# Performance work log

Measured on AMD Instinct MI355X. Metric: run time of the kernel, lower is better.

The kernel has to match this reference:

```python
import jax, jax.numpy as jnp
import numpy as np

B, M, K, D = 16384, 16, 256, 64
T = 1.0


def setup_inputs() -> dict:
    key = jax.random.key(0)
    k1, k2 = jax.random.split(key)
    x = jax.random.normal(k1, (B, M, D), dtype=jnp.float32)
    # nn.init.normal_(self.center, std=0.01)
    center = jax.random.normal(k2, (M, K, D), dtype=jnp.float32) * 0.01
    return {"x": x, "center": center}


def _forward(x, center):
    # x: [B, M, D]; center: [M, K, D]
    x1 = jax.lax.stop_gradient(x)              # x.detach() in the original
    x_sqlen = jnp.sum(x1 * x1, axis=-1)        # [B, M]
    dot = jnp.einsum('mkd,bmd->bmk', center, x1)  # bmm(center, x1) -> [B, M, K]
    c_sqlen = jnp.sum(center * center, axis=-1)   # [M, K]
    dist = c_sqlen[None, :, :] - 2.0 * dot + x_sqlen[:, :, None]  # [B, M, K]
    dist = -jnp.sqrt(dist)
    # softargmax with straight-through estimator
    y_soft = jax.nn.softmax(dist / T, axis=-1)
    label = jnp.argmax(y_soft, axis=-1, keepdims=True)            # [B, M, 1]
    y_hard = jax.nn.one_hot(label[..., 0], K, dtype=dist.dtype)   # [B, M, K]
    assign = y_hard - jax.lax.stop_gradient(y_soft) + y_soft
    # reconstruction: bmm(assign^T(M,B,K), center(M,K,D)) -> [B, M, D]
    recon = jnp.einsum('bmk,mkd->bmd', assign, center)
    return recon, center, label


def reference(x, center):
    return _forward(x, center)
```

## Files before the change

kernel.cpp:

```cpp
#include <hip/hip_runtime.h>
#include <stdint.h>
#include <math.h>

#define B_TOT 16384
#define M_TOT 16
#define K_TOT 256
#define D_TOT 64
#define ROWS_PB 256
#define THREADS 512
#define NCHUNK (B_TOT / ROWS_PB)
#define CAP 2048
#define XERRF 0.0160f
#define SLACK 5.0e-5f

typedef unsigned long long ull;
typedef __attribute__((ext_vector_type(8))) short short8;
typedef __attribute__((ext_vector_type(4))) float f32x4;
typedef __attribute__((ext_vector_type(4))) uint32_t u32x4;

__device__ __forceinline__ uint32_t f32_key(float f) {
  uint32_t u = __float_as_uint(f);
  return (u & 0x80000000u) ? ~u : (u | 0x80000000u);
}
__device__ __forceinline__ ull u64min(ull a, ull b) { return a < b ? a : b; }

__device__ __forceinline__ uint32_t bf16rne(float f) {
  uint32_t u = __float_as_uint(f);
  return (u + 0x7FFFu + ((u >> 16) & 1u)) >> 16;
}
__device__ __forceinline__ uint32_t pack2(float a, float b) {
  return bf16rne(a) | (bf16rne(b) << 16);
}

__device__ __forceinline__ int swz(int row, int c) {
  return row * 128 + ((c * 16) ^ ((row & 7) << 4));
}

__device__ __forceinline__ float xla_hsum16(const float* r) {
#pragma clang fp contract(off)
#pragma clang fp reassociate(off)
  float u[8];
#pragma unroll
  for (int q = 0; q < 8; ++q) u[q] = r[q] + r[q + 8];
  float v[4];
#pragma unroll
  for (int q = 0; q < 4; ++q) v[q] = u[q] + u[q + 4];
  float w0 = v[0] + v[2];
  float w1 = v[1] + v[3];
  return w0 + w1;
}

__device__ __forceinline__ ull exact_key_stream(int k, const float* __restrict__ xrow,
                                                const float* __restrict__ crow,
                                                float csq, float x_sq) {
#pragma clang fp contract(off)
#pragma clang fp reassociate(off)
  const float4* cp = reinterpret_cast<const float4*>(crow);
  const float4* xp = reinterpret_cast<const float4*>(xrow);
  float a[4] = {0.f, 0.f, 0.f, 0.f};
#pragma unroll
  for (int it = 0; it < 4; ++it) {
    float cc[16], xx[16];
#pragma unroll
    for (int q = 0; q < 4; ++q) {
      float4 v = cp[4 * it + q];
      cc[4 * q + 0] = v.x; cc[4 * q + 1] = v.y;
      cc[4 * q + 2] = v.z; cc[4 * q + 3] = v.w;
      float4 w = xp[4 * it + q];
      xx[4 * q + 0] = w.x; xx[4 * q + 1] = w.y;
      xx[4 * q + 2] = w.z; xx[4 * q + 3] = w.w;
    }
#pragma unroll
    for (int L = 0; L < 4; ++L) {
      float m3 = cc[12 + L] * xx[12 + L];
      float s3 = m3 + a[L];
      float m2 = cc[8 + L] * xx[8 + L];
      float s2 = m2 + s3;
      float m1 = cc[4 + L] * xx[4 + L];
      float s1 = m1 + s2;
      float m0 = cc[0 + L] * xx[0 + L];
      a[L] = m0 + s1;
    }
  }
  const float dot = (a[0] + a[1]) + (a[2] + a[3]);
  const float two_dot = 2.0f * dot;
  const float d2 = (csq - two_dot) + x_sq;
  const float s = (float)sqrt((double)d2);
  return (((ull)f32_key(s)) << 32) | (unsigned)k;
}

__global__ __launch_bounds__(THREADS, 4) void mkmeans_fwd(
    const float* __restrict__ x, const float* __restrict__ center,
    float* __restrict__ recon, float* __restrict__ outC, float* __restrict__ outL)
{
#pragma clang fp contract(off)
#pragma clang fp reassociate(off)
  __shared__ __align__(16) char s_xb[ROWS_PB * 128];
  __shared__ __align__(16) char s_cb[K_TOT * 128];
  __shared__ __align__(16) float s_csq[K_TOT];
  __shared__ __align__(16) float s_nch[K_TOT];
  __shared__ float s_xsq[ROWS_PB];
  __shared__ float s_xnorm[ROWS_PB];
  __shared__ float s_cmaxw[4];
  __shared__ ull s_best[ROWS_PB];
  __shared__ uint32_t s_list[CAP];
  __shared__ int s_nc, s_ovf;

  const int t = threadIdx.x;
  const int l = t & 63;
  const int wv = t >> 6;
  const int g = l >> 4;
  const int j = l & 15;
  const int bi = blockIdx.x;
  const int m = bi & (M_TOT - 1);
  const int chunk = bi >> 4;
  const int b0 = chunk * ROWS_PB;

  const float* cmbase = center + (size_t)m * (K_TOT * D_TOT);

  if (t == 0) { s_nc = 0; s_ovf = 0; }

  if (t < ROWS_PB) {
    const float4* xp = reinterpret_cast<const float4*>(
        x + ((size_t)((b0 + t) * M_TOT + m)) * D_TOT);
    float r[16];
#pragma unroll
    for (int mm = 0; mm < 4; ++mm) {
      float q[16];
#pragma unroll
      for (int qq = 0; qq < 4; ++qq) {
        float4 v = xp[4 * mm + qq];
        q[4 * qq + 0] = v.x; q[4 * qq + 1] = v.y;
        q[4 * qq + 2] = v.z; q[4 * qq + 3] = v.w;
      }
#pragma unroll
      for (int jj = 0; jj < 16; ++jj) {
        const float p = q[jj] * q[jj];
        r[jj] = (mm == 0) ? p : (r[jj] + p);
      }
#pragma unroll
      for (int h = 0; h < 2; ++h) {
        u32x4 u = {pack2(q[8 * h + 0], q[8 * h + 1]),
                   pack2(q[8 * h + 2], q[8 * h + 3]),
                   pack2(q[8 * h + 4], q[8 * h + 5]),
                   pack2(q[8 * h + 6], q[8 * h + 7])};
        *reinterpret_cast<u32x4*>(s_xb + swz(t, 2 * mm + h)) = u;
      }
    }
    const float xsq = xla_hsum16(r);
    s_xsq[t] = xsq;
    s_xnorm[t] = sqrtf(xsq) * 1.00001f + 1e-12f;
    s_best[t] = ~0ull;
  } else {
    const int tc = t - ROWS_PB;
    const float4* cp = reinterpret_cast<const float4*>(cmbase + (size_t)tc * D_TOT);
    float4* dst = (chunk == 0)
        ? reinterpret_cast<float4*>(outC + (size_t)m * (K_TOT * D_TOT) + (size_t)tc * D_TOT)
        : nullptr;
    float r[16];
#pragma unroll
    for (int mm = 0; mm < 4; ++mm) {
      float q[16];
#pragma unroll
      for (int qq = 0; qq < 4; ++qq) {
        float4 v = cp[4 * mm + qq];
        if (dst) dst[4 * mm + qq] = v;
        q[4 * qq + 0] = v.x; q[4 * qq + 1] = v.y;
        q[4 * qq + 2] = v.z; q[4 * qq + 3] = v.w;
      }
#pragma unroll
      for (int jj = 0; jj < 16; ++jj) {
        const float p = q[jj] * q[jj];
        r[jj] = (mm == 0) ? p : (r[jj] + p);
      }
#pragma unroll
      for (int h = 0; h < 2; ++h) {
        u32x4 u = {pack2(q[8 * h + 0], q[8 * h + 1]),
                   pack2(q[8 * h + 2], q[8 * h + 3]),
                   pack2(q[8 * h + 4], q[8 * h + 5]),
                   pack2(q[8 * h + 6], q[8 * h + 7])};
        *reinterpret_cast<u32x4*>(s_cb + swz(tc, 2 * mm + h)) = u;
      }
    }
    const float csq = xla_hsum16(r);
    s_csq[tc] = csq;
    s_nch[tc] = -0.5f * csq;
    float cs = sqrtf(csq) * 1.00001f + 1e-12f;
#pragma unroll
    for (int off = 1; off < 64; off <<= 1)
      cs = fmaxf(cs, __shfl_xor(cs, off, 64));
    if (l == 0) s_cmaxw[wv - 4] = cs;
  }
  __syncthreads();

  const int row0 = wv * 32 + j;
  const int row1 = row0 + 16;
  short8 bfr[2][2];
#pragma unroll
  for (int rg = 0; rg < 2; ++rg) {
    const int row = rg ? row1 : row0;
#pragma unroll
    for (int ks = 0; ks < 2; ++ks)
      bfr[rg][ks] = *reinterpret_cast<const short8*>(s_xb + swz(row, ks * 4 + g));
  }
  const float cmax = fmaxf(fmaxf(s_cmaxw[0], s_cmaxw[1]),
                           fmaxf(s_cmaxw[2], s_cmaxw[3]));
  float Wa[2];
  Wa[0] = XERRF * s_xnorm[row0] * cmax + 0.5f * SLACK;
  Wa[1] = XERRF * s_xnorm[row1] * cmax + 0.5f * SLACK;

  float m1[2] = {-3.0e38f, -3.0e38f};
  ull mk[2] = {0ull, 0ull};
#pragma unroll
  for (int T = 0; T < 16; ++T) {
    short8 af0 = *reinterpret_cast<const short8*>(s_cb + swz(T * 16 + j, 0 + g));
    short8 af1 = *reinterpret_cast<const short8*>(s_cb + swz(T * 16 + j, 4 + g));
    const f32x4 nch = *reinterpret_cast<const f32x4*>(&s_nch[T * 16 + g * 4]);
#pragma unroll
    for (int rg = 0; rg < 2; ++rg) {
      f32x4 a = __builtin_amdgcn_mfma_f32_16x16x32_bf16(af0, bfr[rg][0], nch, 0, 0, 0);
      a = __builtin_amdgcn_mfma_f32_16x16x32_bf16(af1, bfr[rg][1], a, 0, 0, 0);
      const float tmax = fmaxf(fmaxf(a[0], a[1]), fmaxf(a[2], a[3]));
      const bool rs = tmax > m1[rg] + Wa[rg];
      const float m1n = fmaxf(m1[rg], tmax);
      const float thr = m1n - Wa[rg];
      uint32_t bits = 0u;
      bits |= (a[0] >= thr) ? 1u : 0u;
      bits |= (a[1] >= thr) ? 2u : 0u;
      bits |= (a[2] >= thr) ? 4u : 0u;
      bits |= (a[3] >= thr) ? 8u : 0u;
      mk[rg] = (rs ? 0ull : mk[rg]) | (((ull)bits) << (4 * T));
      m1[rg] = m1n;
    }
  }

#pragma unroll
  for (int rg = 0; rg < 2; ++rg) {
    float v = m1[rg];
    v = fmaxf(v, __shfl_xor(v, 16, 64));
    v = fmaxf(v, __shfl_xor(v, 32, 64));
    const int row = rg ? row1 : row0;
    if (m1[rg] >= v - Wa[rg]) {
      ull msk = mk[rg];
      while (msk) {
        const int p = __builtin_ctzll(msk);
        msk &= msk - 1;
        const int k = (p >> 2) * 16 + g * 4 + (p & 3);
        const int idx = atomicAdd(&s_nc, 1);
        if (idx < CAP)
          s_list[idx] = ((uint32_t)row << 16) | (uint32_t)k;
        else
          s_ovf = 1;
      }
    }
  }
  __syncthreads();

  if (!s_ovf) {
    const int n = s_nc;
#pragma unroll 1
    for (int i = t; i < n; i += THREADS) {
      const uint32_t e = s_list[i];
      const int row = (int)(e >> 16);
      const int k = (int)(e & 0xffffu);
      const float* xrow = x + ((size_t)((b0 + row) * M_TOT + m)) * D_TOT;
      const float* crow = cmbase + (size_t)k * D_TOT;
      const ull key = exact_key_stream(k, xrow, crow, s_csq[k], s_xsq[row]);
      atomicMin(&s_best[row], key);
    }
  } else if (t < ROWS_PB) {
    const float* xrow = x + ((size_t)((b0 + t) * M_TOT + m)) * D_TOT;
    ull best = ~0ull;
#pragma unroll 1
    for (int k = 0; k < K_TOT; ++k)
      best = u64min(best, exact_key_stream(k, xrow, cmbase + (size_t)k * D_TOT,
                                           s_csq[k], s_xsq[t]));
    s_best[t] = best;
  }
  __syncthreads();

  if (t < ROWS_PB)
    outL[(size_t)(b0 + t) * M_TOT + m] = (float)(uint32_t)(s_best[t] & 0xffffffffull);

  const float4* cm4 = reinterpret_cast<const float4*>(cmbase);
  float4* rec4 = reinterpret_cast<float4*>(recon);
#pragma unroll
  for (int it = 0; it < (ROWS_PB * 16) / THREADS; ++it) {
    const int slot = it * THREADS + t;
    const int row = slot >> 4, ch = slot & 15;
    const int kst = (int)(s_best[row] & 0xffffffffull);
    rec4[((size_t)((b0 + row) * M_TOT + m)) * 16 + ch] = cm4[kst * 16 + ch];
  }
}

extern "C" void kernel_launch(void* const* d_in, const int* in_sizes, int n_in,
                              void* d_out, int out_size, void* d_ws, size_t ws_size,
                              hipStream_t stream) {
  const float* x = (const float*)d_in[0];
  const float* center = (const float*)d_in[1];
  float* recon = (float*)d_out;
  float* outC = recon + (size_t)B_TOT * M_TOT * D_TOT;
  float* outL = outC + (size_t)M_TOT * K_TOT * D_TOT;

  mkmeans_fwd<<<dim3(NCHUNK * M_TOT), dim3(THREADS), 0, stream>>>(x, center, recon, outC, outL);
}
```

Before: 211.2 us.

## Double rows per block, load x fragments from global, filter by per-tile bf16 max

Each block now handles 512 rows instead of 256. The bf16 x staging buffer in shared memory is removed, and each thread loads and packs its MFMA B fragments straight from global memory. The running-max candidate reset is replaced by storing a rounded-up bf16 maximum per 16-key tile, and the candidate list is then filtered per tile against the final row maximum. This is meant to amortize the per-block center staging over more rows and cut LDS traffic. In exchange it uses more registers (occupancy hint drops to 2), reads x from global twice, and may produce more candidates, so CAP is raised.

```diff
diff --git a/kernel.cpp b/kernel.cpp
--- a/kernel.cpp
+++ b/kernel.cpp
@@ -6,10 +6,10 @@
 #define M_TOT 16
 #define K_TOT 256
 #define D_TOT 64
-#define ROWS_PB 256
+#define ROWS_PB 512
 #define THREADS 512
 #define NCHUNK (B_TOT / ROWS_PB)
-#define CAP 2048
+#define CAP 3072
 #define XERRF 0.0160f
 #define SLACK 5.0e-5f
 
@@ -30,6 +30,10 @@
 }
 __device__ __forceinline__ uint32_t pack2(float a, float b) {
   return bf16rne(a) | (bf16rne(b) << 16);
+}
+__device__ __forceinline__ uint32_t bf16up(float f) {
+  uint32_t u = __float_as_uint(f);
+  return (((int)u >= 0) ? (u + 0xFFFFu) : u) >> 16;
 }
 
 __device__ __forceinline__ int swz(int row, int c) {
@@ -89,13 +93,12 @@
   return (((ull)f32_key(s)) << 32) | (unsigned)k;
 }
 
-__global__ __launch_bounds__(THREADS, 4) void mkmeans_fwd(
+__global__ __launch_bounds__(THREADS, 2) void mkmeans_fwd(
     const float* __restrict__ x, const float* __restrict__ center,
     float* __restrict__ recon, float* __restrict__ outC, float* __restrict__ outL)
 {
 #pragma clang fp contract(off)
 #pragma clang fp reassociate(off)
-  __shared__ __align__(16) char s_xb[ROWS_PB * 128];
   __shared__ __align__(16) char s_cb[K_TOT * 128];
   __shared__ __align__(16) float s_csq[K_TOT];
   __shared__ __align__(16) float s_nch[K_TOT];
@@ -119,17 +122,21 @@
   const float* cmbase = center + (size_t)m * (K_TOT * D_TOT);
 
   if (t == 0) { s_nc = 0; s_ovf = 0; }
-
-  if (t < ROWS_PB) {
-    const float4* xp = reinterpret_cast<const float4*>(
-        x + ((size_t)((b0 + t) * M_TOT + m)) * D_TOT);
+  s_best[t] = ~0ull;
+
+  if (t < K_TOT) {
+    const float4* cp = reinterpret_cast<const float4*>(cmbase + (size_t)t * D_TOT);
+    float4* dst = (chunk == 0)
+        ? reinterpret_cast<float4*>(outC + (size_t)m * (K_TOT * D_TOT) + (size_t)t * D_TOT)
+        : nullptr;
     float r[16];
 #pragma unroll
     for (int mm = 0; mm < 4; ++mm) {
       float q[16];
 #pragma unroll
       for (int qq = 0; qq < 4; ++qq) {
-        float4 v = xp[4 * mm + qq];
+        float4 v = cp[4 * mm + qq];
+        if (dst) dst[4 * mm + qq] = v;
         q[4 * qq + 0] = v.x; q[4 * qq + 1] = v.y;
         q[4 * qq + 2] = v.z; q[4 * qq + 3] = v.w;
       }
@@ -144,113 +151,117 @@
                    pack2(q[8 * h + 2], q[8 * h + 3]),
                    pack2(q[8 * h + 4], q[8 * h + 5]),
                    pack2(q[8 * h + 6], q[8 * h + 7])};
-        *reinterpret_cast<u32x4*>(s_xb + swz(t, 2 * mm + h)) = u;
+        *reinterpret_cast<u32x4*>(s_cb + swz(t, 2 * mm + h)) = u;
+      }
+    }
+    const float csq = xla_hsum16(r);
+    s_csq[t] = csq;
+    s_nch[t] = -0.5f * csq;
+    float cs = sqrtf(csq) * 1.00001f + 1e-12f;
+#pragma unroll
+    for (int off = 1; off < 64; off <<= 1)
+      cs = fmaxf(cs, __shfl_xor(cs, off, 64));
+    if (l == 0) s_cmaxw[wv] = cs;
+  }
+
+  {
+    const float4* xp = reinterpret_cast<const float4*>(
+        x + ((size_t)((b0 + t) * M_TOT + m)) * D_TOT);
+    float r[16];
+#pragma unroll
+    for (int mm = 0; mm < 4; ++mm) {
+      float q[16];
+#pragma unroll
+      for (int qq = 0; qq < 4; ++qq) {
+        float4 v = xp[4 * mm + qq];
+        q[4 * qq + 0] = v.x; q[4 * qq + 1] = v.y;
+        q[4 * qq + 2] = v.z; q[4 * qq + 3] = v.w;
+      }
+#pragma unroll
+      for (int jj = 0; jj < 16; ++jj) {
+        const float p = q[jj] * q[jj];
+        r[jj] = (mm == 0) ? p : (r[jj] + p);
       }
     }
     const float xsq = xla_hsum16(r);
     s_xsq[t] = xsq;
     s_xnorm[t] = sqrtf(xsq) * 1.00001f + 1e-12f;
-    s_best[t] = ~0ull;
-  } else {
-    const int tc = t - ROWS_PB;
-    const float4* cp = reinterpret_cast<const float4*>(cmbase + (size_t)tc * D_TOT);
-    float4* dst = (chunk == 0)
-        ? reinterpret_cast<float4*>(outC + (size_t)m * (K_TOT * D_TOT) + (size_t)tc * D_TOT)
-        : nullptr;
-    float r[16];
-#pragma unroll
-    for (int mm = 0; mm < 4; ++mm) {
-      float q[16];
-#pragma unroll
-      for (int qq = 0; qq < 4; ++qq) {
-        float4 v = cp[4 * mm + qq];
-        if (dst) dst[4 * mm + qq] = v;
-        q[4 * qq + 0] = v.x; q[4 * qq + 1] = v.y;
-        q[4 * qq + 2] = v.z; q[4 * qq + 3] = v.w;
-      }
-#pragma unroll
-      for (int jj = 0; jj < 16; ++jj) {
-        const float p = q[jj] * q[jj];
-        r[jj] = (mm == 0) ? p : (r[jj] + p);
-      }
-#pragma unroll
-      for (int h = 0; h < 2; ++h) {
-        u32x4 u = {pack2(q[8 * h + 0], q[8 * h + 1]),
-                   pack2(q[8 * h + 2], q[8 * h + 3]),
-                   pack2(q[8 * h + 4], q[8 * h + 5]),
-                   pack2(q[8 * h + 6], q[8 * h + 7])};
-        *reinterpret_cast<u32x4*>(s_cb + swz(tc, 2 * mm + h)) = u;
-      }
-    }
-    const float csq = xla_hsum16(r);
-    s_csq[tc] = csq;
-    s_nch[tc] = -0.5f * csq;
-    float cs = sqrtf(csq) * 1.00001f + 1e-12f;
-#pragma unroll
-    for (int off = 1; off < 64; off <<= 1)
-      cs = fmaxf(cs, __shfl_xor(cs, off, 64));
-    if (l == 0) s_cmaxw[wv - 4] = cs;
+  }
+
+  short8 bfr[4][2];
+#pragma unroll
+  for (int rg = 0; rg < 4; ++rg) {
+    const int row = wv * 64 + rg * 16 + j;
+    const float4* xr4 = reinterpret_cast<const float4*>(
+        x + ((size_t)((b0 + row) * M_TOT + m)) * D_TOT);
+#pragma unroll
+    for (int ks = 0; ks < 2; ++ks) {
+      const int c = ks * 4 + g;
+      const float4 f0 = xr4[2 * c];
+      const float4 f1 = xr4[2 * c + 1];
+      u32x4 u = {pack2(f0.x, f0.y), pack2(f0.z, f0.w),
+                 pack2(f1.x, f1.y), pack2(f1.z, f1.w)};
+      bfr[rg][ks] = *reinterpret_cast<short8*>(&u);
+    }
   }
   __syncthreads();
 
-  const int row0 = wv * 32 + j;
-  const int row1 = row0 + 16;
-  short8 bfr[2][2];
-#pragma unroll
-  for (int rg = 0; rg < 2; ++rg) {
-    const int row = rg ? row1 : row0;
-#pragma unroll
-    for (int ks = 0; ks < 2; ++ks)
-      bfr[rg][ks] = *reinterpret_cast<const short8*>(s_xb + swz(row, ks * 4 + g));
-  }
   const float cmax = fmaxf(fmaxf(s_cmaxw[0], s_cmaxw[1]),
                            fmaxf(s_cmaxw[2], s_cmaxw[3]));
-  float Wa[2];
-  Wa[0] = XERRF * s_xnorm[row0] * cmax + 0.5f * SLACK;
-  Wa[1] = XERRF * s_xnorm[row1] * cmax + 0.5f * SLACK;
-
-  float m1[2] = {-3.0e38f, -3.0e38f};
-  ull mk[2] = {0ull, 0ull};
+  float Wa[4];
+#pragma unroll
+  for (int rg = 0; rg < 4; ++rg)
+    Wa[rg] = XERRF * s_xnorm[wv * 64 + rg * 16 + j] * cmax + 0.5f * SLACK;
+
+  float m1[4] = {-3.0e38f, -3.0e38f, -3.0e38f, -3.0e38f};
+  ull mk[4] = {0ull, 0ull, 0ull, 0ull};
+  uint32_t tb[4][8];
 #pragma unroll
   for (int T = 0; T < 16; ++T) {
-    short8 af0 = *reinterpret_cast<const short8*>(s_cb + swz(T * 16 + j, 0 + g));
-    short8 af1 = *reinterpret_cast<const short8*>(s_cb + swz(T * 16 + j, 4 + g));
+    const short8 af0 = *reinterpret_cast<const short8*>(s_cb + swz(T * 16 + j, g));
+    const short8 af1 = *reinterpret_cast<const short8*>(s_cb + swz(T * 16 + j, 4 + g));
     const f32x4 nch = *reinterpret_cast<const f32x4*>(&s_nch[T * 16 + g * 4]);
 #pragma unroll
-    for (int rg = 0; rg < 2; ++rg) {
+    for (int rg = 0; rg < 4; ++rg) {
       f32x4 a = __builtin_amdgcn_mfma_f32_16x16x32_bf16(af0, bfr[rg][0], nch, 0, 0, 0);
       a = __builtin_amdgcn_mfma_f32_16x16x32_bf16(af1, bfr[rg][1], a, 0, 0, 0);
       const float tmax = fmaxf(fmaxf(a[0], a[1]), fmaxf(a[2], a[3]));
-      const bool rs = tmax > m1[rg] + Wa[rg];
-      const float m1n = fmaxf(m1[rg], tmax);
-      const float thr = m1n - Wa[rg];
+      const float thr = tmax - Wa[rg];
       uint32_t bits = 0u;
       bits |= (a[0] >= thr) ? 1u : 0u;
       bits |= (a[1] >= thr) ? 2u : 0u;
       bits |= (a[2] >= thr) ? 4u : 0u;
       bits |= (a[3] >= thr) ? 8u : 0u;
-      mk[rg] = (rs ? 0ull : mk[rg]) | (((ull)bits) << (4 * T));
-      m1[rg] = m1n;
-    }
-  }
-
-#pragma unroll
-  for (int rg = 0; rg < 2; ++rg) {
+      mk[rg] |= ((ull)bits) << (4 * T);
+      m1[rg] = fmaxf(m1[rg], tmax);
+      const uint32_t h = bf16up(tmax);
+      if (T & 1) tb[rg][T >> 1] |= h << 16; else tb[rg][T >> 1] = h;
+    }
+  }
+
+#pragma unroll
+  for (int rg = 0; rg < 4; ++rg) {
     float v = m1[rg];
     v = fmaxf(v, __shfl_xor(v, 16, 64));
     v = fmaxf(v, __shfl_xor(v, 32, 64));
-    const int row = rg ? row1 : row0;
-    if (m1[rg] >= v - Wa[rg]) {
-      ull msk = mk[rg];
-      while (msk) {
-        const int p = __builtin_ctzll(msk);
-        msk &= msk - 1;
-        const int k = (p >> 2) * 16 + g * 4 + (p & 3);
-        const int idx = atomicAdd(&s_nc, 1);
-        if (idx < CAP)
-          s_list[idx] = ((uint32_t)row << 16) | (uint32_t)k;
-        else
-          s_ovf = 1;
+    const float cut = v - Wa[rg];
+    const int row = wv * 64 + rg * 16 + j;
+#pragma unroll
+    for (int T = 0; T < 16; ++T) {
+      const uint32_t h = (tb[rg][T >> 1] >> ((T & 1) * 16)) & 0xFFFFu;
+      const float tmaxbf = __uint_as_float(h << 16);
+      if (tmaxbf >= cut) {
+        uint32_t bits = (uint32_t)((mk[rg] >> (4 * T)) & 0xFull);
+        while (bits) {
+          const int i = __builtin_ctz(bits);
+          bits &= bits - 1;
+          const int k = T * 16 + g * 4 + i;
+          const int idx = atomicAdd(&s_nc, 1);
+          if (idx < CAP)
+            s_list[idx] = ((uint32_t)row << 16) | (uint32_t)k;
+          else
+            s_ovf = 1;
+        }
       }
     }
   }
@@ -268,7 +279,7 @@
       const ull key = exact_key_stream(k, xrow, crow, s_csq[k], s_xsq[row]);
       atomicMin(&s_best[row], key);
     }
-  } else if (t < ROWS_PB) {
+  } else {
     const float* xrow = x + ((size_t)((b0 + t) * M_TOT + m)) * D_TOT;
     ull best = ~0ull;
 #pragma unroll 1
@@ -279,8 +290,7 @@
   }
   __syncthreads();
 
-  if (t < ROWS_PB)
-    outL[(size_t)(b0 + t) * M_TOT + m] = (float)(uint32_t)(s_best[t] & 0xffffffffull);
+  outL[(size_t)(b0 + t) * M_TOT + m] = (float)(uint32_t)(s_best[t] & 0xffffffffull);
 
   const float4* cm4 = reinterpret_cast<const float4*>(cmbase);
   float4* rec4 = reinterpret_cast<float4*>(recon);
```

Result: slower. 233.4 us (+10.5%).

## Recompute MFMA scores in second pass with per-center error bound for tighter candidate filter

Applied to the files above, without the earlier changes.

Replaces the single-pass running-max bitmask candidate filter with two MFMA passes. The first finds the row maximum and the second recomputes scores and emits candidates against a threshold that uses each center's norm instead of the global max norm. This should shrink the candidate list and the exact fp32 rescoring work. The x fragments are now loaded straight from global memory into registers, dropping the shared x buffer, and the candidate capacity is raised. The cost is doubled MFMA and LDS reads, plus shared atomics issued per candidate inside the unrolled loop.

```diff
diff --git a/kernel.cpp b/kernel.cpp
--- a/kernel.cpp
+++ b/kernel.cpp
@@ -9,8 +9,8 @@
 #define ROWS_PB 256
 #define THREADS 512
 #define NCHUNK (B_TOT / ROWS_PB)
-#define CAP 2048
-#define XERRF 0.0160f
+#define CAP 3072
+#define XS 8.0e-3f
 #define SLACK 5.0e-5f
 
 typedef unsigned long long ull;
@@ -95,10 +95,10 @@
 {
 #pragma clang fp contract(off)
 #pragma clang fp reassociate(off)
-  __shared__ __align__(16) char s_xb[ROWS_PB * 128];
   __shared__ __align__(16) char s_cb[K_TOT * 128];
   __shared__ __align__(16) float s_csq[K_TOT];
   __shared__ __align__(16) float s_nch[K_TOT];
+  __shared__ __align__(16) float s_csqrt[K_TOT];
   __shared__ float s_xsq[ROWS_PB];
   __shared__ float s_xnorm[ROWS_PB];
   __shared__ float s_cmaxw[4];
@@ -137,14 +137,6 @@
       for (int jj = 0; jj < 16; ++jj) {
         const float p = q[jj] * q[jj];
         r[jj] = (mm == 0) ? p : (r[jj] + p);
-      }
-#pragma unroll
-      for (int h = 0; h < 2; ++h) {
-        u32x4 u = {pack2(q[8 * h + 0], q[8 * h + 1]),
-                   pack2(q[8 * h + 2], q[8 * h + 3]),
-                   pack2(q[8 * h + 4], q[8 * h + 5]),
-                   pack2(q[8 * h + 6], q[8 * h + 7])};
-        *reinterpret_cast<u32x4*>(s_xb + swz(t, 2 * mm + h)) = u;
       }
     }
     const float xsq = xla_hsum16(r);
@@ -185,72 +177,80 @@
     const float csq = xla_hsum16(r);
     s_csq[tc] = csq;
     s_nch[tc] = -0.5f * csq;
-    float cs = sqrtf(csq) * 1.00001f + 1e-12f;
+    const float cs = sqrtf(csq) * 1.00001f + 1e-12f;
+    s_csqrt[tc] = cs;
+    float cw = cs;
 #pragma unroll
     for (int off = 1; off < 64; off <<= 1)
-      cs = fmaxf(cs, __shfl_xor(cs, off, 64));
-    if (l == 0) s_cmaxw[wv - 4] = cs;
+      cw = fmaxf(cw, __shfl_xor(cw, off, 64));
+    if (l == 0) s_cmaxw[wv - 4] = cw;
+  }
+
+  short8 bfr[2][2];
+#pragma unroll
+  for (int rg = 0; rg < 2; ++rg) {
+    const int row = wv * 32 + rg * 16 + j;
+    const float4* xr4 = reinterpret_cast<const float4*>(
+        x + ((size_t)((b0 + row) * M_TOT + m)) * D_TOT);
+#pragma unroll
+    for (int ks = 0; ks < 2; ++ks) {
+      const int c = ks * 4 + g;
+      const float4 f0 = xr4[2 * c];
+      const float4 f1 = xr4[2 * c + 1];
+      u32x4 u = {pack2(f0.x, f0.y), pack2(f0.z, f0.w),
+                 pack2(f1.x, f1.y), pack2(f1.z, f1.w)};
+      bfr[rg][ks] = *reinterpret_cast<short8*>(&u);
+    }
   }
   __syncthreads();
 
-  const int row0 = wv * 32 + j;
-  const int row1 = row0 + 16;
-  short8 bfr[2][2];
-#pragma unroll
-  for (int rg = 0; rg < 2; ++rg) {
-    const int row = rg ? row1 : row0;
-#pragma unroll
-    for (int ks = 0; ks < 2; ++ks)
-      bfr[rg][ks] = *reinterpret_cast<const short8*>(s_xb + swz(row, ks * 4 + g));
-  }
-  const float cmax = fmaxf(fmaxf(s_cmaxw[0], s_cmaxw[1]),
-                           fmaxf(s_cmaxw[2], s_cmaxw[3]));
-  float Wa[2];
-  Wa[0] = XERRF * s_xnorm[row0] * cmax + 0.5f * SLACK;
-  Wa[1] = XERRF * s_xnorm[row1] * cmax + 0.5f * SLACK;
-
   float m1[2] = {-3.0e38f, -3.0e38f};
-  ull mk[2] = {0ull, 0ull};
 #pragma unroll
   for (int T = 0; T < 16; ++T) {
-    short8 af0 = *reinterpret_cast<const short8*>(s_cb + swz(T * 16 + j, 0 + g));
-    short8 af1 = *reinterpret_cast<const short8*>(s_cb + swz(T * 16 + j, 4 + g));
+    const short8 af0 = *reinterpret_cast<const short8*>(s_cb + swz(T * 16 + j, g));
+    const short8 af1 = *reinterpret_cast<const short8*>(s_cb + swz(T * 16 + j, 4 + g));
     const f32x4 nch = *reinterpret_cast<const f32x4*>(&s_nch[T * 16 + g * 4]);
 #pragma unroll
     for (int rg = 0; rg < 2; ++rg) {
       f32x4 a = __builtin_amdgcn_mfma_f32_16x16x32_bf16(af0, bfr[rg][0], nch, 0, 0, 0);
       a = __builtin_amdgcn_mfma_f32_16x16x32_bf16(af1, bfr[rg][1], a, 0, 0, 0);
-      const float tmax = fmaxf(fmaxf(a[0], a[1]), fmaxf(a[2], a[3]));
-      const bool rs = tmax > m1[rg] + Wa[rg];
-      const float m1n = fmaxf(m1[rg], tmax);
-      const float thr = m1n - Wa[rg];
-      uint32_t bits = 0u;
-      bits |= (a[0] >= thr) ? 1u : 0u;
-      bits |= (a[1] >= thr) ? 2u : 0u;
-      bits |= (a[2] >= thr) ? 4u : 0u;
-      bits |= (a[3] >= thr) ? 8u : 0u;
-      mk[rg] = (rs ? 0ull : mk[rg]) | (((ull)bits) << (4 * T));
-      m1[rg] = m1n;
-    }
-  }
-
+      m1[rg] = fmaxf(m1[rg], fmaxf(fmaxf(a[0], a[1]), fmaxf(a[2], a[3])));
+    }
+  }
+
+  const float cmax = fmaxf(fmaxf(s_cmaxw[0], s_cmaxw[1]),
+                           fmaxf(s_cmaxw[2], s_cmaxw[3]));
+  float base[2], xw[2];
 #pragma unroll
   for (int rg = 0; rg < 2; ++rg) {
     float v = m1[rg];
     v = fmaxf(v, __shfl_xor(v, 16, 64));
     v = fmaxf(v, __shfl_xor(v, 32, 64));
-    const int row = rg ? row1 : row0;
-    if (m1[rg] >= v - Wa[rg]) {
-      ull msk = mk[rg];
-      while (msk) {
-        const int p = __builtin_ctzll(msk);
-        msk &= msk - 1;
-        const int k = (p >> 2) * 16 + g * 4 + (p & 3);
-        const int idx = atomicAdd(&s_nc, 1);
-        if (idx < CAP)
-          s_list[idx] = ((uint32_t)row << 16) | (uint32_t)k;
-        else
-          s_ovf = 1;
+    xw[rg] = XS * s_xnorm[wv * 32 + rg * 16 + j];
+    base[rg] = v - xw[rg] * cmax - SLACK;
+  }
+
+#pragma unroll
+  for (int T = 0; T < 16; ++T) {
+    const short8 af0 = *reinterpret_cast<const short8*>(s_cb + swz(T * 16 + j, g));
+    const short8 af1 = *reinterpret_cast<const short8*>(s_cb + swz(T * 16 + j, 4 + g));
+    const f32x4 nch = *reinterpret_cast<const f32x4*>(&s_nch[T * 16 + g * 4]);
+    const f32x4 cs = *reinterpret_cast<const f32x4*>(&s_csqrt[T * 16 + g * 4]);
+#pragma unroll
+    for (int rg = 0; rg < 2; ++rg) {
+      f32x4 a = __builtin_amdgcn_mfma_f32_16x16x32_bf16(af0, bfr[rg][0], nch, 0, 0, 0);
+      a = __builtin_amdgcn_mfma_f32_16x16x32_bf16(af1, bfr[rg][1], a, 0, 0, 0);
+      const int row = wv * 32 + rg * 16 + j;
+#pragma unroll
+      for (int i = 0; i < 4; ++i) {
+        const float thr = fmaf(-xw[rg], cs[i], base[rg]);
+        if (a[i] >= thr) {
+          const int idx = atomicAdd(&s_nc, 1);
+          if (idx < CAP)
+            s_list[idx] = ((uint32_t)row << 16) | (uint32_t)(T * 16 + g * 4 + i);
+          else
+            s_ovf = 1;
+        }
       }
     }
   }
```

Result: faster. 175.6 us (-16.8%).
